# Optimization experiments

Measured on AMD Instinct MI355X. Metric: run time of the kernel, lower is better.

## Reference

```python
import jax, jax.numpy as jnp
import numpy as np

EPS = 1e-5
L = 512
P1 = 64  # patch_num + 1
B = 512
H = 2048


def layernorm2d(x, g, b):
    # LayerNorm over the last two dims [P1, L]
    mu = jnp.mean(x, axis=(-2, -1), keepdims=True)
    var = jnp.mean(jnp.square(x - mu), axis=(-2, -1), keepdims=True)
    return (x - mu) * jax.lax.rsqrt(var + EPS) * g + b


def freq_filter(x, w):
    # rfft(x) * rfft(w) then irfft, all with ortho normalization
    X = jnp.fft.rfft(x, axis=-1, norm='ortho')          # [B, P1, L//2+1]
    W = jnp.fft.rfft(w, axis=-1, norm='ortho')          # [1, L//2+1]
    return jnp.fft.irfft(X * W, n=L, axis=-1, norm='ortho')


def setup_inputs() -> dict:
    key = jax.random.key(0)
    ks = jax.random.split(key, 4)
    x = jax.random.normal(ks[0], (B, P1, L), dtype=jnp.float32)
    w = 0.02 * jax.random.normal(ks[1], (1, L), dtype=jnp.float32)
    w1 = jax.random.normal(ks[2], (L, H), dtype=jnp.float32) * (1.0 / np.sqrt(L))
    b1 = jnp.zeros((H,), jnp.float32)
    w2 = jax.random.normal(ks[3], (H, L), dtype=jnp.float32) * (1.0 / np.sqrt(H))
    b2 = jnp.zeros((L,), jnp.float32)
    return {
        'x': x, 'w': w,
        'ln1_w': jnp.ones((P1, L), jnp.float32), 'ln1_b': jnp.zeros((P1, L), jnp.float32),
        'ln2_w': jnp.ones((P1, L), jnp.float32), 'ln2_b': jnp.zeros((P1, L), jnp.float32),
        'w1': w1, 'b1': b1, 'w2': w2, 'b2': b2,
    }


def reference(x, w, ln1_w, ln1_b, ln2_w, ln2_b, w1, b1, w2, b2):
    res = x
    h = layernorm2d(x, ln1_w, ln1_b)
    h = freq_filter(h, w)
    # dropout is identity in inference
    h = layernorm2d(h, ln2_w, ln2_b)
    # PositionwiseFeedForward: Linear -> ReLU -> (dropout) -> Linear
    h = jax.nn.relu(jnp.einsum('bpl,lh->bph', h, w1) + b1)
    h = jnp.einsum('bph,hl->bpl', h, w2) + b2
    return h + res
```

## Files before the change

kernel.cpp:

```cpp
#include <hip/hip_runtime.h>

typedef __bf16  bf16x8 __attribute__((ext_vector_type(8)));
typedef float   f32x16 __attribute__((ext_vector_type(16)));
typedef unsigned short u16;

__device__ __forceinline__ u16 f2bf(float f) {
  union { float f; unsigned u32; } c; c.f = f;
  unsigned r = c.u32 + 0x7fffu + ((c.u32 >> 16) & 1u);
  return (u16)(r >> 16);
}
__device__ __forceinline__ float bf2f(u16 u) {
  union { unsigned u32; float f; } c; c.u32 = (unsigned)u << 16; return c.f;
}

__device__ __forceinline__ void async16(const void* g, void* l) {
  __builtin_amdgcn_global_load_lds(
      (const __attribute__((address_space(1))) unsigned*)g,
      (__attribute__((address_space(3))) unsigned*)l, 16, 0, 0);
}

__global__ __launch_bounds__(256) void build_ct(const float* __restrict__ w,
                                                u16* __restrict__ ct) {
  int idx = blockIdx.x * 256 + threadIdx.x;
  int n = idx >> 9, k = idx & 511;
  float v = w[(n - k) & 511] * 0.04419417382415922f;
  ct[idx] = f2bf(v);
}

__global__ __launch_bounds__(256) void transpose_w(const float* __restrict__ in,
                                                   u16* __restrict__ out,
                                                   int R, int C) {
  __shared__ float tile[32][33];
  int bx = blockIdx.x * 32;
  int by = blockIdx.y * 32;
  int tx = threadIdx.x & 31, ty = threadIdx.x >> 5;
#pragma unroll
  for (int r = ty; r < 32; r += 8)
    tile[r][tx] = in[(size_t)(by + r) * C + bx + tx];
  __syncthreads();
#pragma unroll
  for (int r = ty; r < 32; r += 8)
    out[(size_t)(bx + r) * R + by + tx] = f2bf(tile[tx][r]);
}

__global__ __launch_bounds__(512, 2) void ln_f32(const float* __restrict__ x,
                                                 const float* __restrict__ g,
                                                 const float* __restrict__ beta,
                                                 u16* __restrict__ out) {
  const int tid = threadIdx.x;
  const size_t base = (size_t)blockIdx.x * 32768;
  float4 v[16];
  float s = 0.f, ss = 0.f;
#pragma unroll
  for (int j = 0; j < 16; ++j) {
    v[j] = *(const float4*)(x + base + tid * 4 + j * 2048);
    s  += v[j].x + v[j].y + v[j].z + v[j].w;
    ss += v[j].x * v[j].x + v[j].y * v[j].y + v[j].z * v[j].z + v[j].w * v[j].w;
  }
#pragma unroll
  for (int off = 32; off > 0; off >>= 1) {
    s += __shfl_down(s, off, 64);
    ss += __shfl_down(ss, off, 64);
  }
  __shared__ float red[16];
  int wave = tid >> 6, lane = tid & 63;
  if (lane == 0) { red[wave] = s; red[8 + wave] = ss; }
  __syncthreads();
  float S = 0.f, SS = 0.f;
#pragma unroll
  for (int wv = 0; wv < 8; ++wv) { S += red[wv]; SS += red[8 + wv]; }
  const float inv = 1.0f / 32768.0f;
  float mu = S * inv;
  float rs = rsqrtf(SS * inv - mu * mu + 1e-5f);
#pragma unroll
  for (int j = 0; j < 16; ++j) {
    const int i = tid * 4 + j * 2048;
    float4 gv = *(const float4*)(g + i);
    float4 bv = *(const float4*)(beta + i);
    uint2 o;
    o.x = (unsigned)f2bf((v[j].x - mu) * rs * gv.x + bv.x) |
          ((unsigned)f2bf((v[j].y - mu) * rs * gv.y + bv.y) << 16);
    o.y = (unsigned)f2bf((v[j].z - mu) * rs * gv.z + bv.z) |
          ((unsigned)f2bf((v[j].w - mu) * rs * gv.w + bv.w) << 16);
    *(uint2*)(out + base + i) = o;
  }
}

__global__ __launch_bounds__(512, 2) void ln_bf16(const u16* __restrict__ x,
                                                  const float* __restrict__ g,
                                                  const float* __restrict__ beta,
                                                  u16* __restrict__ out) {
  const int tid = threadIdx.x;
  const size_t base = (size_t)blockIdx.x * 32768;
  uint4 v[8];
  float s = 0.f, ss = 0.f;
#pragma unroll
  for (int j = 0; j < 8; ++j) {
    v[j] = *(const uint4*)(x + base + tid * 8 + j * 4096);
    const unsigned* a = &v[j].x;
#pragma unroll
    for (int t = 0; t < 4; ++t) {
      float lo = bf2f((u16)(a[t] & 0xffff)), hi = bf2f((u16)(a[t] >> 16));
      s += lo + hi; ss += lo * lo + hi * hi;
    }
  }
#pragma unroll
  for (int off = 32; off > 0; off >>= 1) {
    s += __shfl_down(s, off, 64);
    ss += __shfl_down(ss, off, 64);
  }
  __shared__ float red[16];
  int wave = tid >> 6, lane = tid & 63;
  if (lane == 0) { red[wave] = s; red[8 + wave] = ss; }
  __syncthreads();
  float S = 0.f, SS = 0.f;
#pragma unroll
  for (int wv = 0; wv < 8; ++wv) { S += red[wv]; SS += red[8 + wv]; }
  const float inv = 1.0f / 32768.0f;
  float mu = S * inv;
  float rs = rsqrtf(SS * inv - mu * mu + 1e-5f);
#pragma unroll
  for (int j = 0; j < 8; ++j) {
    const int i = tid * 8 + j * 4096;
    const unsigned* a = &v[j].x;
    uint4 o;
    unsigned* ov = &o.x;
#pragma unroll
    for (int t = 0; t < 4; ++t) {
      float lo = bf2f((u16)(a[t] & 0xffff)), hi = bf2f((u16)(a[t] >> 16));
      float glo = g[i + 2 * t], ghi = g[i + 2 * t + 1];
      float blo = beta[i + 2 * t], bhi = beta[i + 2 * t + 1];
      ov[t] = (unsigned)f2bf((lo - mu) * rs * glo + blo) |
              ((unsigned)f2bf((hi - mu) * rs * ghi + bhi) << 16);
    }
    *(uint4*)(out + base + i) = o;
  }
}

template <int MODE>
__global__ __launch_bounds__(512, 2) void gemm_bt(
    const u16* __restrict__ A, const u16* __restrict__ Bt,
    const float* __restrict__ bias, const float* __restrict__ resid,
    float* __restrict__ Cf, u16* __restrict__ Cb,
    int M, int N, int K, int MT) {
  __shared__ u16 As[16384];
  __shared__ u16 Bs[16384];

  const int tid  = threadIdx.x;
  const int lane = tid & 63;
  const int wave = tid >> 6;
  const int l31  = lane & 31, hi = lane >> 5;
  const int wr = wave >> 2, wc = wave & 3;

  const int nwg = gridDim.x;
  const int q = nwg >> 3, r8 = nwg & 7;
  const int xcd = blockIdx.x & 7, loc = blockIdx.x >> 3;
  const int wgid =
      (xcd < r8 ? xcd * (q + 1) : r8 * (q + 1) + (xcd - r8) * q) + loc;
  const int bm = wgid % MT, bn = wgid / MT;
  const int m0 = bm * 256, n0 = bn * 256;
  (void)M;

  const u16* ag = A  + (size_t)(m0 + (tid >> 1)) * K + (tid & 1) * 8;
  const u16* bg = Bt + (size_t)(n0 + (tid >> 1)) * K + (tid & 1) * 8;

  const int aoff = (wr * 128 + l31) * 16 + hi * 8;
  const int boff = (wc * 64  + l31) * 16 + hi * 8;

  f32x16 acc[4][2];
#pragma unroll
  for (int m = 0; m < 4; ++m)
#pragma unroll
    for (int n = 0; n < 2; ++n)
#pragma unroll
      for (int i = 0; i < 16; ++i) acc[m][n][i] = 0.f;

  const int NT = K >> 4;

  async16(ag,      As + tid * 8);
  async16(bg,      Bs + tid * 8);
  async16(ag + 16, As + 4096 + tid * 8);
  async16(bg + 16, Bs + 4096 + tid * 8);
  asm volatile("s_waitcnt vmcnt(2)" ::: "memory");
  __builtin_amdgcn_sched_barrier(0);
  __builtin_amdgcn_s_barrier();

  for (int u = 0; u < NT; ++u) {
    const int bb = (u & 3) * 4096;
    bf16x8 av[4], bv[2];
#pragma unroll
    for (int m = 0; m < 4; ++m)
      av[m] = *(const bf16x8*)&As[bb + aoff + m * 512];
#pragma unroll
    for (int n = 0; n < 2; ++n)
      bv[n] = *(const bf16x8*)&Bs[bb + boff + n * 512];
    if (u + 2 < NT) {
      const int sb = ((u + 2) & 3) * 4096 + tid * 8;
      async16(ag + (size_t)(u + 2) * 16, As + sb);
      async16(bg + (size_t)(u + 2) * 16, Bs + sb);
    }
    __builtin_amdgcn_s_barrier();
    asm volatile("s_waitcnt lgkmcnt(0)" ::: "memory");
    __builtin_amdgcn_sched_barrier(0);
    __builtin_amdgcn_s_setprio(1);
#pragma unroll
    for (int m = 0; m < 4; ++m)
#pragma unroll
      for (int n = 0; n < 2; ++n)
        acc[m][n] = __builtin_amdgcn_mfma_f32_32x32x16_bf16(av[m], bv[n],
                                                            acc[m][n], 0, 0, 0);
    __builtin_amdgcn_s_setprio(0);
    __builtin_amdgcn_sched_barrier(0);
    if (u + 2 < NT) asm volatile("s_waitcnt vmcnt(2)" ::: "memory");
    else            asm volatile("s_waitcnt vmcnt(0)" ::: "memory");
    __builtin_amdgcn_sched_barrier(0);
    __builtin_amdgcn_s_barrier();
  }

#pragma unroll
  for (int n = 0; n < 2; ++n) {
    const int col = n0 + wc * 64 + n * 32 + l31;
    float bj = 0.f;
    if (MODE >= 1) bj = bias[col];
#pragma unroll
    for (int m = 0; m < 4; ++m) {
      const int row0 = m0 + wr * 128 + m * 32 + hi * 4;
#pragma unroll
      for (int g = 0; g < 4; ++g)
#pragma unroll
        for (int t = 0; t < 4; ++t) {
          float v = acc[m][n][g * 4 + t] + bj;
          if (MODE == 1) v = fmaxf(v, 0.f);
          const size_t idx = (size_t)(row0 + g * 8 + t) * N + col;
          if (MODE == 2) { v += resid[idx]; Cf[idx] = v; }
          else           Cb[idx] = f2bf(v);
        }
    }
  }
}

extern "C" void kernel_launch(void* const* d_in, const int* in_sizes, int n_in,
                              void* d_out, int out_size, void* d_ws,
                              size_t ws_size, hipStream_t stream) {
  const float* x    = (const float*)d_in[0];
  const float* w    = (const float*)d_in[1];
  const float* ln1w = (const float*)d_in[2];
  const float* ln1b = (const float*)d_in[3];
  const float* ln2w = (const float*)d_in[4];
  const float* ln2b = (const float*)d_in[5];
  const float* w1   = (const float*)d_in[6];
  const float* b1   = (const float*)d_in[7];
  const float* w2   = (const float*)d_in[8];
  const float* b2   = (const float*)d_in[9];
  float* out = (float*)d_out;

  char* ws = (char*)d_ws;
  u16*   y   = (u16*)(ws);
  u16*   h1  = (u16*)(ws);
  u16*   h2  = (u16*)(ws + 33554432);
  u16*   h3  = (u16*)(ws + 134217728);
  u16*   ct  = (u16*)(ws + 167772160);
  u16*   w1t = (u16*)(ws + 168296448);
  u16*   w2t = (u16*)(ws + 170393600);

  build_ct<<<1024, 256, 0, stream>>>(w, ct);
  transpose_w<<<dim3(64, 16), 256, 0, stream>>>(w1, w1t, 512, 2048);
  transpose_w<<<dim3(16, 64), 256, 0, stream>>>(w2, w2t, 2048, 512);

  ln_f32<<<512, 512, 0, stream>>>(x, ln1w, ln1b, h1);
  gemm_bt<0><<<256, 512, 0, stream>>>(h1, ct, nullptr, nullptr,
                                      nullptr, h2, 32768, 512, 512, 128);
  ln_bf16<<<512, 512, 0, stream>>>(h2, ln2w, ln2b, h3);
  gemm_bt<1><<<1024, 512, 0, stream>>>(h3, w1t, b1, nullptr,
                                       nullptr, y, 32768, 2048, 512, 128);
  gemm_bt<2><<<256, 512, 0, stream>>>(y, w2t, b2, x,
                                      out, nullptr, 32768, 512, 2048, 128);
}
```

Measured before the change: 401.1 us.

## Restructure bf16 GEMM with 64-wide K tiles, swizzled LDS, and quadrant pipelining

Rewrites the GEMM main loop to use 16x16x32 bf16 MFMAs with K-steps of 64 instead of 16, double-buffered in a larger LDS allocation (128 KB total). The LDS layout is XOR-swizzled to avoid bank conflicts, and each K-step is split into four quadrant phases. Each phase interleaves async global-to-LDS staging of the next tile with MFMA work on the current one. The aim is fewer barriers per unit of work and better overlap of memory with compute. In exchange it uses more LDS, which may limit occupancy to one block per CU despite launch_bounds(512,2), and the synchronisation is more intricate.

Result: no change. 400.5 us (-0.1%).

```diff
diff --git a/kernel.cpp b/kernel.cpp
--- a/kernel.cpp
+++ b/kernel.cpp
@@ -1,7 +1,7 @@
 #include <hip/hip_runtime.h>
 
 typedef __bf16  bf16x8 __attribute__((ext_vector_type(8)));
-typedef float   f32x16 __attribute__((ext_vector_type(16)));
+typedef float   f32x4  __attribute__((ext_vector_type(4)));
 typedef unsigned short u16;
 
 __device__ __forceinline__ u16 f2bf(float f) {
@@ -143,100 +143,157 @@
     const float* __restrict__ bias, const float* __restrict__ resid,
     float* __restrict__ Cf, u16* __restrict__ Cb,
     int M, int N, int K, int MT) {
-  __shared__ u16 As[16384];
-  __shared__ u16 Bs[16384];
+  __shared__ u16 As[32768];
+  __shared__ u16 Bs[32768];
 
   const int tid  = threadIdx.x;
   const int lane = tid & 63;
   const int wave = tid >> 6;
-  const int l31  = lane & 31, hi = lane >> 5;
+  const int l16  = lane & 15, quad = lane >> 4;
   const int wr = wave >> 2, wc = wave & 3;
 
   const int nwg = gridDim.x;
-  const int q = nwg >> 3, r8 = nwg & 7;
+  const int q8 = nwg >> 3, r8 = nwg & 7;
   const int xcd = blockIdx.x & 7, loc = blockIdx.x >> 3;
   const int wgid =
-      (xcd < r8 ? xcd * (q + 1) : r8 * (q + 1) + (xcd - r8) * q) + loc;
+      (xcd < r8 ? xcd * (q8 + 1) : r8 * (q8 + 1) + (xcd - r8) * q8) + loc;
   const int bm = wgid % MT, bn = wgid / MT;
   const int m0 = bm * 256, n0 = bn * 256;
   (void)M;
 
-  const u16* ag = A  + (size_t)(m0 + (tid >> 1)) * K + (tid & 1) * 8;
-  const u16* bg = Bt + (size_t)(n0 + (tid >> 1)) * K + (tid & 1) * 8;
-
-  const int aoff = (wr * 128 + l31) * 16 + hi * 8;
-  const int boff = (wc * 64  + l31) * 16 + hi * 8;
-
-  f32x16 acc[4][2];
-#pragma unroll
-  for (int m = 0; m < 4; ++m)
-#pragma unroll
-    for (int n = 0; n < 2; ++n)
-#pragma unroll
-      for (int i = 0; i < 16; ++i) acc[m][n][i] = 0.f;
-
-  const int NT = K >> 4;
-
-  async16(ag,      As + tid * 8);
-  async16(bg,      Bs + tid * 8);
-  async16(ag + 16, As + 4096 + tid * 8);
-  async16(bg + 16, Bs + 4096 + tid * 8);
-  asm volatile("s_waitcnt vmcnt(2)" ::: "memory");
-  __builtin_amdgcn_sched_barrier(0);
-  __builtin_amdgcn_s_barrier();
-
-  for (int u = 0; u < NT; ++u) {
-    const int bb = (u & 3) * 4096;
-    bf16x8 av[4], bv[2];
-#pragma unroll
-    for (int m = 0; m < 4; ++m)
-      av[m] = *(const bf16x8*)&As[bb + aoff + m * 512];
-#pragma unroll
-    for (int n = 0; n < 2; ++n)
-      bv[n] = *(const bf16x8*)&Bs[bb + boff + n * 512];
-    if (u + 2 < NT) {
-      const int sb = ((u + 2) & 3) * 4096 + tid * 8;
-      async16(ag + (size_t)(u + 2) * 16, As + sb);
-      async16(bg + (size_t)(u + 2) * 16, Bs + sb);
-    }
-    __builtin_amdgcn_s_barrier();
-    asm volatile("s_waitcnt lgkmcnt(0)" ::: "memory");
-    __builtin_amdgcn_sched_barrier(0);
-    __builtin_amdgcn_s_setprio(1);
-#pragma unroll
-    for (int m = 0; m < 4; ++m)
-#pragma unroll
-      for (int n = 0; n < 2; ++n)
-        acc[m][n] = __builtin_amdgcn_mfma_f32_32x32x16_bf16(av[m], bv[n],
-                                                            acc[m][n], 0, 0, 0);
+  const int srow   = tid >> 3;
+  const int grp    = tid >> 8;
+  const int srow32 = srow & 31;
+  const int gch    = ((tid & 7) ^ (srow & 7)) * 8;
+  const u16* agb = A  + (size_t)(m0 + srow) * K + gch;
+  const u16* bgb = Bt + (size_t)(n0 + grp * 64 + srow32) * K + gch;
+  const int adst = tid * 8;
+  const int bdst = grp * 4096 + (tid & 255) * 8;
+
+#define STAGE_A(t1, qm) {                                                   \
+    const u16* g_ = agb + (size_t)(qm) * 64 * K + (t1) * 64;                \
+    u16* d_ = As + (((t1) & 1) << 14) + (qm) * 4096 + adst;                 \
+    async16(g_, d_);                                                        \
+    async16(g_ + (size_t)128 * K, d_ + 8192); }
+#define STAGE_B(t1, qn) {                                                   \
+    const u16* g_ = bgb + (size_t)(qn) * 32 * K + (t1) * 64;                \
+    u16* d_ = Bs + (((t1) & 1) << 14) + (qn) * 2048 + bdst;                 \
+    async16(g_, d_);                                                        \
+    async16(g_ + (size_t)128 * K, d_ + 8192); }
+
+  const int arow = wr * 8192 + l16 * 64;
+  const int brow = wc * 4096 + l16 * 64;
+  const int sw0 = ((0 + quad) ^ (l16 & 7)) * 8;
+  const int sw1 = ((4 + quad) ^ (l16 & 7)) * 8;
+
+  bf16x8 av[4][2], bv[2][2][2];
+  f32x4 acc[8][4];
+#pragma unroll
+  for (int i = 0; i < 8; ++i)
+#pragma unroll
+    for (int j = 0; j < 4; ++j) acc[i][j] = (f32x4){0.f, 0.f, 0.f, 0.f};
+
+#define LDA(qm) {                                                           \
+    const int ab = (buf << 14) + (qm) * 4096 + arow;                        \
+    _Pragma("unroll")                                                       \
+    for (int m_ = 0; m_ < 4; ++m_) {                                        \
+      av[m_][0] = *(const bf16x8*)&As[ab + m_ * 1024 + sw0];                \
+      av[m_][1] = *(const bf16x8*)&As[ab + m_ * 1024 + sw1];                \
+    } }
+#define LDB(qn) {                                                           \
+    const int bb = (buf << 14) + (qn) * 2048 + brow;                        \
+    _Pragma("unroll")                                                       \
+    for (int n_ = 0; n_ < 2; ++n_) {                                        \
+      bv[qn][n_][0] = *(const bf16x8*)&Bs[bb + n_ * 1024 + sw0];            \
+      bv[qn][n_][1] = *(const bf16x8*)&Bs[bb + n_ * 1024 + sw1];            \
+    } }
+#define MFMA_Q(qm, qn)                                                      \
+    __builtin_amdgcn_s_setprio(1);                                          \
+    _Pragma("unroll")                                                       \
+    for (int m_ = 0; m_ < 4; ++m_) {                                        \
+      _Pragma("unroll")                                                     \
+      for (int n_ = 0; n_ < 2; ++n_) {                                      \
+        acc[(qm)*4+m_][(qn)*2+n_] = __builtin_amdgcn_mfma_f32_16x16x32_bf16(\
+            av[m_][0], bv[qn][n_][0], acc[(qm)*4+m_][(qn)*2+n_], 0, 0, 0);  \
+        acc[(qm)*4+m_][(qn)*2+n_] = __builtin_amdgcn_mfma_f32_16x16x32_bf16(\
+            av[m_][1], bv[qn][n_][1], acc[(qm)*4+m_][(qn)*2+n_], 0, 0, 0);  \
+      } }                                                                   \
     __builtin_amdgcn_s_setprio(0);
-    __builtin_amdgcn_sched_barrier(0);
-    if (u + 2 < NT) asm volatile("s_waitcnt vmcnt(2)" ::: "memory");
-    else            asm volatile("s_waitcnt vmcnt(0)" ::: "memory");
-    __builtin_amdgcn_sched_barrier(0);
-    __builtin_amdgcn_s_barrier();
-  }
-
-#pragma unroll
-  for (int n = 0; n < 2; ++n) {
-    const int col = n0 + wc * 64 + n * 32 + l31;
-    float bj = 0.f;
-    if (MODE >= 1) bj = bias[col];
-#pragma unroll
-    for (int m = 0; m < 4; ++m) {
-      const int row0 = m0 + wr * 128 + m * 32 + hi * 4;
-#pragma unroll
-      for (int g = 0; g < 4; ++g)
-#pragma unroll
-        for (int t = 0; t < 4; ++t) {
-          float v = acc[m][n][g * 4 + t] + bj;
-          if (MODE == 1) v = fmaxf(v, 0.f);
-          const size_t idx = (size_t)(row0 + g * 8 + t) * N + col;
-          if (MODE == 2) { v += resid[idx]; Cf[idx] = v; }
-          else           Cb[idx] = f2bf(v);
+
+#define SB    __builtin_amdgcn_sched_barrier(0)
+#define BAR   __builtin_amdgcn_s_barrier()
+#define LGKM0 asm volatile("s_waitcnt lgkmcnt(0)" ::: "memory")
+#define VM(n) asm volatile("s_waitcnt vmcnt(" #n ")" ::: "memory")
+
+  const int NT = K >> 6;
+
+  STAGE_A(0, 0); STAGE_B(0, 0); STAGE_B(0, 1); STAGE_A(0, 1);
+  VM(4);
+  SB; BAR;
+
+  for (int t = 0; t < NT; ++t) {
+    const int buf = t & 1;
+    const bool more = (t + 1) < NT;
+    LDA(0); LDB(0);
+    if (more) STAGE_A(t + 1, 0);
+    BAR; LGKM0; SB;
+    MFMA_Q(0, 0);
+    SB;
+    if (more) VM(4); else VM(2);
+    SB; BAR;
+    LDB(1);
+    if (more) STAGE_B(t + 1, 0);
+    BAR; LGKM0; SB;
+    MFMA_Q(0, 1);
+    SB;
+    if (more) VM(4); else VM(0);
+    SB; BAR;
+    LDA(1);
+    if (more) STAGE_B(t + 1, 1);
+    BAR; LGKM0; SB;
+    MFMA_Q(1, 0);
+    SB; BAR;
+    if (more) STAGE_A(t + 1, 1);
+    BAR; SB;
+    MFMA_Q(1, 1);
+    SB;
+    if (more) VM(4);
+    SB; BAR;
+  }
+
+#undef STAGE_A
+#undef STAGE_B
+#undef LDA
+#undef LDB
+#undef MFMA_Q
+#undef SB
+#undef BAR
+#undef LGKM0
+#undef VM
+
+#pragma unroll
+  for (int qn = 0; qn < 2; ++qn)
+#pragma unroll
+    for (int n = 0; n < 2; ++n) {
+      const int col = n0 + wc * 64 + qn * 32 + n * 16 + l16;
+      float bj = 0.f;
+      if (MODE >= 1) bj = bias[col];
+#pragma unroll
+      for (int qm = 0; qm < 2; ++qm)
+#pragma unroll
+        for (int m = 0; m < 4; ++m) {
+          const int row0 = m0 + wr * 128 + qm * 64 + m * 16 + quad * 4;
+          f32x4 a = acc[qm * 4 + m][qn * 2 + n];
+#pragma unroll
+          for (int r = 0; r < 4; ++r) {
+            float v = a[r] + bj;
+            if (MODE == 1) v = fmaxf(v, 0.f);
+            const size_t idx = (size_t)(row0 + r) * N + col;
+            if (MODE == 2) { v += resid[idx]; Cf[idx] = v; }
+            else           Cb[idx] = f2bf(v);
+          }
         }
     }
-  }
 }
 
 extern "C" void kernel_launch(void* const* d_in, const int* in_sizes, int n_in,
```
